# Performance work log

Hardware: AMD Instinct MI355X
Metric: run time of the kernel (lower is better)

## Reference

```python
import jax, jax.numpy as jnp
import numpy as np

B, N_IN, HID, N_OUT = 1024, 512, 64, 256


def setup_inputs() -> dict:
    key = jax.random.key(0)
    ks = jax.random.split(key, 10)
    s = 0.02
    return {
        "x": jax.random.normal(ks[0], (B, N_IN), dtype=jnp.float32),
        "ln_gamma": jnp.ones((N_IN,), dtype=jnp.float32),
        "ln_beta": jnp.zeros((N_IN,), dtype=jnp.float32),
        "Wq": jax.random.normal(ks[1], (N_IN, HID * N_OUT), dtype=jnp.float32) * s,
        "bq": jnp.zeros((HID * N_OUT,), dtype=jnp.float32),
        "Wk": jax.random.normal(ks[2], (N_IN, HID * N_OUT), dtype=jnp.float32) * s,
        "bk": jnp.zeros((HID * N_OUT,), dtype=jnp.float32),
        "Wv": jax.random.normal(ks[3], (N_IN, HID * N_OUT), dtype=jnp.float32) * s,
        "bv": jnp.zeros((HID * N_OUT,), dtype=jnp.float32),
        "Wo": jax.random.normal(ks[4], (HID, N_OUT), dtype=jnp.float32) * s,
        "bo": jnp.zeros((N_OUT,), dtype=jnp.float32),
    }


def reference(x, ln_gamma, ln_beta, Wq, bq, Wk, bk, Wv, bv, Wo, bo):
    # LayerNorm over last dim (input_shape)
    mu = jnp.mean(x, axis=-1, keepdims=True)
    var = jnp.mean(jnp.square(x - mu), axis=-1, keepdims=True)
    h = (x - mu) / jnp.sqrt(var + 1e-5) * ln_gamma + ln_beta  # (B, 512)

    # QKV projections, then view as (B, N_OUT, HID)
    q = (h @ Wq + bq).reshape(B, N_OUT, HID)
    k = (h @ Wk + bk).reshape(B, N_OUT, HID)
    v = (h @ Wv + bv).reshape(B, N_OUT, HID)

    # Single-head scaled dot-product attention over length N_OUT
    w = jnp.einsum("bqc,bkc->bqk", q, k) * (HID ** -0.5)
    w = jax.nn.softmax(w, axis=2)
    a = jnp.einsum("bqk,bkc->bqc", w, v)  # (B, N_OUT, HID)

    # Output projection, ReLU, negate -> seminegative contact map
    out = jax.nn.relu(a @ Wo + bo)  # (B, N_OUT, N_OUT)
    return -out
```

## Files before the change

kernel.cpp:

```cpp
#include <hip/hip_runtime.h>
#include <hip/hip_fp16.h>

typedef _Float16 h4_t __attribute__((ext_vector_type(4)));
typedef _Float16 h8_t __attribute__((ext_vector_type(8)));
typedef float f4_t __attribute__((ext_vector_type(4)));

#define B_SZ 1024
#define N_IN 512
#define HID 64
#define N_OUT 256
#define QKN (N_OUT * HID)

__global__ __launch_bounds__(256) void k_ln(const float* __restrict__ x,
                                            const float* __restrict__ gamma,
                                            const float* __restrict__ beta,
                                            _Float16* __restrict__ h16) {
    int tid = threadIdx.x;
    int wave = tid >> 6, lane = tid & 63;
    int row = blockIdx.x * 4 + wave;
    const float4* xr = (const float4*)(x + (size_t)row * N_IN);
    float4 a = xr[lane];
    float4 b = xr[lane + 64];
    float s = a.x + a.y + a.z + a.w + b.x + b.y + b.z + b.w;
    float sq = a.x * a.x + a.y * a.y + a.z * a.z + a.w * a.w +
               b.x * b.x + b.y * b.y + b.z * b.z + b.w * b.w;
    for (int off = 1; off < 64; off <<= 1) {
        s += __shfl_xor(s, off);
        sq += __shfl_xor(sq, off);
    }
    float mean = s * (1.0f / N_IN);
    float var = sq * (1.0f / N_IN) - mean * mean;
    float rstd = rsqrtf(var + 1e-5f);
    float4 g0 = ((const float4*)gamma)[lane];
    float4 g1 = ((const float4*)gamma)[lane + 64];
    float4 e0 = ((const float4*)beta)[lane];
    float4 e1 = ((const float4*)beta)[lane + 64];
    h4_t o0 = {(_Float16)((a.x - mean) * rstd * g0.x + e0.x),
               (_Float16)((a.y - mean) * rstd * g0.y + e0.y),
               (_Float16)((a.z - mean) * rstd * g0.z + e0.z),
               (_Float16)((a.w - mean) * rstd * g0.w + e0.w)};
    h4_t o1 = {(_Float16)((b.x - mean) * rstd * g1.x + e1.x),
               (_Float16)((b.y - mean) * rstd * g1.y + e1.y),
               (_Float16)((b.z - mean) * rstd * g1.z + e1.z),
               (_Float16)((b.w - mean) * rstd * g1.w + e1.w)};
    h4_t* hr = (h4_t*)(h16 + (size_t)row * N_IN);
    hr[lane] = o0;
    hr[lane + 64] = o1;
}

__global__ __launch_bounds__(256) void k_wt(const float* __restrict__ Wq,
                                            const float* __restrict__ Wk,
                                            const float* __restrict__ Wv,
                                            _Float16* __restrict__ wt) {
    __shared__ _Float16 t[64][65];
    const float* W = blockIdx.z == 0 ? Wq : (blockIdx.z == 1 ? Wk : Wv);
    _Float16* out = wt + (size_t)blockIdx.z * ((size_t)QKN * N_IN);
    int n0 = blockIdx.x * 64, k0 = blockIdx.y * 64;
    int c = threadIdx.x & 63, rq = threadIdx.x >> 6;
    for (int i = 0; i < 16; i++) {
        int r = i * 4 + rq;
        t[r][c] = (_Float16)W[(size_t)(k0 + r) * QKN + n0 + c];
    }
    __syncthreads();
    for (int i = 0; i < 16; i++) {
        int r = i * 4 + rq;
        out[(size_t)(n0 + r) * N_IN + k0 + c] = t[c][r];
    }
}

__global__ __launch_bounds__(256) void k_wo(const float* __restrict__ Wo,
                                            _Float16* __restrict__ wo16) {
    int id = blockIdx.x * 256 + threadIdx.x;
    int hid = id >> 8, no = id & 255;
    wo16[(hid >> 2) * 1024 + no * 4 + (hid & 3)] = (_Float16)Wo[id];
}

__global__ __launch_bounds__(256) void k_qkv(const _Float16* __restrict__ h16,
                                             const _Float16* __restrict__ wt,
                                             const float* __restrict__ bq,
                                             const float* __restrict__ bk,
                                             const float* __restrict__ bv,
                                             _Float16* __restrict__ qkv) {
    __shared__ _Float16 As[128 * 32];
    __shared__ _Float16 Bs[128 * 32];
    int z = blockIdx.z;
    const _Float16* Wb = wt + (size_t)z * ((size_t)QKN * N_IN);
    const float* bias = z == 0 ? bq : (z == 1 ? bk : bv);
    float qscale = (z == 0) ? 0.125f * 1.44269504088896f : 1.0f;
    _Float16* out = qkv + (size_t)z * ((size_t)B_SZ * QKN);
    int m0 = blockIdx.x * 128, n0 = blockIdx.y * 128;
    int tid = threadIdx.x, lane = tid & 63, w = tid >> 6;
    int wm = w & 1, wn = w >> 1;
    int col16 = lane & 15, quad = lane >> 4;
    f4_t acc[4][4] = {};
    for (int kk = 0; kk < N_IN; kk += 32) {
        __syncthreads();
        for (int c = 0; c < 2; c++) {
            int idx = (w * 2 + c) * 512 + lane * 8;
            int row = idx >> 5, col = idx & 31;
            __builtin_amdgcn_global_load_lds(
                (const __attribute__((address_space(1))) void*)(h16 + (size_t)(m0 + row) * N_IN + kk + col),
                (__attribute__((address_space(3))) void*)(As + (w * 2 + c) * 512),
                16, 0, 0);
            __builtin_amdgcn_global_load_lds(
                (const __attribute__((address_space(1))) void*)(Wb + (size_t)(n0 + row) * N_IN + kk + col),
                (__attribute__((address_space(3))) void*)(Bs + (w * 2 + c) * 512),
                16, 0, 0);
        }
        __syncthreads();
        h8_t af[4], bf[4];
        for (int mt = 0; mt < 4; mt++)
            af[mt] = *(const h8_t*)(As + (wm * 64 + mt * 16 + col16) * 32 + quad * 8);
        for (int nt = 0; nt < 4; nt++)
            bf[nt] = *(const h8_t*)(Bs + (wn * 64 + nt * 16 + col16) * 32 + quad * 8);
        for (int mt = 0; mt < 4; mt++)
            for (int nt = 0; nt < 4; nt++)
                acc[mt][nt] = __builtin_amdgcn_mfma_f32_16x16x32_f16(af[mt], bf[nt], acc[mt][nt], 0, 0, 0);
    }
    for (int nt = 0; nt < 4; nt++) {
        int n = n0 + wn * 64 + nt * 16 + col16;
        float bb = bias[n];
        for (int mt = 0; mt < 4; mt++) {
            int mbase = m0 + wm * 64 + mt * 16 + quad * 4;
            for (int r = 0; r < 4; r++)
                out[(size_t)(mbase + r) * QKN + n] = (_Float16)((acc[mt][nt][r] + bb) * qscale);
        }
    }
}

__global__ __launch_bounds__(256, 3) void k_attn(const _Float16* __restrict__ qkv,
                                                 const _Float16* __restrict__ wo16,
                                                 const float* __restrict__ bo,
                                                 float* __restrict__ out) {
    __shared__ _Float16 vt[64 * 258];
    int b = blockIdx.x;
    int tid = threadIdx.x, lane = tid & 63, w = tid >> 6;
    int col16 = lane & 15, quad = lane >> 4;
    const _Float16* qb = qkv + (size_t)b * QKN;
    const _Float16* kb = qkv + (size_t)(B_SZ + b) * QKN;
    const _Float16* vb = qkv + (size_t)(2 * B_SZ + b) * QKN;

    for (int it = 0; it < 4; it++) {
        int id = it * 256 + tid;
        int kg = id & 63, hg = id >> 6;
        h4_t r0 = *(const h4_t*)(vb + (kg * 4 + 0) * 64 + hg * 4);
        h4_t r1 = *(const h4_t*)(vb + (kg * 4 + 1) * 64 + hg * 4);
        h4_t r2 = *(const h4_t*)(vb + (kg * 4 + 2) * 64 + hg * 4);
        h4_t r3 = *(const h4_t*)(vb + (kg * 4 + 3) * 64 + hg * 4);
        for (int j = 0; j < 4; j++) {
            h4_t wv = {r0[j], r1[j], r2[j], r3[j]};
            *(h4_t*)(vt + kg * 258 + (hg * 4 + j) * 4) = wv;
        }
    }

    h8_t qf[4][2];
    int qbase = w * 64;
    for (int qt = 0; qt < 4; qt++)
        for (int ki = 0; ki < 2; ki++)
            qf[qt][ki] = *(const h8_t*)(qb + (size_t)(qbase + qt * 16 + col16) * 64 + ki * 32 + quad * 8);

    __syncthreads();

    f4_t o[4][4] = {};
    float lrun[4] = {0.f, 0.f, 0.f, 0.f};

    for (int kc = 0; kc < 16; kc++) {
        h8_t kf[2];
        for (int ki = 0; ki < 2; ki++)
            kf[ki] = *(const h8_t*)(kb + (size_t)(kc * 16 + col16) * 64 + ki * 32 + quad * 8);
        h4_t vf[4];
        for (int mt = 0; mt < 4; mt++)
            vf[mt] = *(const h4_t*)(vt + (kc * 4 + quad) * 258 + (mt * 16 + col16) * 4);
        for (int qt = 0; qt < 4; qt++) {
            f4_t st = {};
            st = __builtin_amdgcn_mfma_f32_16x16x32_f16(kf[0], qf[qt][0], st, 0, 0, 0);
            st = __builtin_amdgcn_mfma_f32_16x16x32_f16(kf[1], qf[qt][1], st, 0, 0, 0);
            float p0 = exp2f(st[0]), p1 = exp2f(st[1]);
            float p2 = exp2f(st[2]), p3 = exp2f(st[3]);
            lrun[qt] += (p0 + p1) + (p2 + p3);
            h4_t pf = {(_Float16)p0, (_Float16)p1, (_Float16)p2, (_Float16)p3};
            for (int mt = 0; mt < 4; mt++)
                o[mt][qt] = __builtin_amdgcn_mfma_f32_16x16x16f16(vf[mt], pf, o[mt][qt], 0, 0, 0);
        }
    }

    h4_t af[4][4];
    for (int qt = 0; qt < 4; qt++) {
        float l = lrun[qt];
        l += __shfl_xor(l, 16);
        l += __shfl_xor(l, 32);
        float rl = 1.0f / l;
        for (int hk = 0; hk < 4; hk++) {
            f4_t t = o[hk][qt];
            af[qt][hk] = (h4_t){(_Float16)(t[0] * rl), (_Float16)(t[1] * rl),
                                (_Float16)(t[2] * rl), (_Float16)(t[3] * rl)};
        }
    }

    float* outb = out + (size_t)b * (N_OUT * N_OUT);
    for (int nc = 0; nc < 16; nc++) {
        int nb = nc * 16;
        h4_t wf[4];
        for (int hk = 0; hk < 4; hk++)
            wf[hk] = *(const h4_t*)(wo16 + (hk * 4 + quad) * 1024 + (nb + col16) * 4);
        float4 b4 = *(const float4*)(bo + nb + quad * 4);
        for (int qt = 0; qt < 4; qt++) {
            f4_t a = {};
            for (int hk = 0; hk < 4; hk++)
                a = __builtin_amdgcn_mfma_f32_16x16x16f16(wf[hk], af[qt][hk], a, 0, 0, 0);
            float4 res;
            res.x = fminf(-(a[0] + b4.x), 0.f);
            res.y = fminf(-(a[1] + b4.y), 0.f);
            res.z = fminf(-(a[2] + b4.z), 0.f);
            res.w = fminf(-(a[3] + b4.w), 0.f);
            *(float4*)(outb + (size_t)(qbase + qt * 16 + col16) * N_OUT + nb + quad * 4) = res;
        }
    }
}

extern "C" void kernel_launch(void* const* d_in, const int* in_sizes, int n_in,
                              void* d_out, int out_size, void* d_ws, size_t ws_size,
                              hipStream_t stream) {
    const float* x = (const float*)d_in[0];
    const float* gamma = (const float*)d_in[1];
    const float* beta = (const float*)d_in[2];
    const float* Wq = (const float*)d_in[3];
    const float* bq = (const float*)d_in[4];
    const float* Wk = (const float*)d_in[5];
    const float* bk = (const float*)d_in[6];
    const float* Wv = (const float*)d_in[7];
    const float* bv = (const float*)d_in[8];
    const float* Wo = (const float*)d_in[9];
    const float* bo = (const float*)d_in[10];
    float* out = (float*)d_out;

    _Float16* h16 = (_Float16*)d_ws;
    _Float16* wt16 = h16 + (size_t)B_SZ * N_IN;
    _Float16* qkv16 = wt16 + (size_t)3 * QKN * N_IN;
    _Float16* wo16 = qkv16 + (size_t)3 * B_SZ * QKN;

    k_ln<<<dim3(B_SZ / 4), 256, 0, stream>>>(x, gamma, beta, h16);
    k_wo<<<dim3(QKN / 256), 256, 0, stream>>>(Wo, wo16);
    k_wt<<<dim3(QKN / 64, N_IN / 64, 3), 256, 0, stream>>>(Wq, Wk, Wv, wt16);
    k_qkv<<<dim3(B_SZ / 128, QKN / 128, 3), 256, 0, stream>>>(h16, wt16, bq, bk, bv, qkv16);
    k_attn<<<dim3(B_SZ), 256, 0, stream>>>(qkv16, wo16, bo, out);
}
```

Measured before the change: 533.1 us.

## Vectorize weight transpose and QKV epilogue stores, swap grid mapping

The weight transpose kernel now reads float4 rows and writes 4-wide half vectors instead of scalar elements. The QKV GEMM swaps the MFMA operand order, so each lane holds four consecutive output columns. The epilogue can then issue 8-byte vector stores along the contiguous dimension, with float4 bias loads. The grid is also reordered so consecutive blocks walk the N dimension and share the same activation tile. The scalar transposed LDS writes in the transpose kernel may cause more bank conflicts.

```diff
diff --git a/kernel.cpp b/kernel.cpp
--- a/kernel.cpp
+++ b/kernel.cpp
@@ -56,15 +56,26 @@
     const float* W = blockIdx.z == 0 ? Wq : (blockIdx.z == 1 ? Wk : Wv);
     _Float16* out = wt + (size_t)blockIdx.z * ((size_t)QKN * N_IN);
     int n0 = blockIdx.x * 64, k0 = blockIdx.y * 64;
-    int c = threadIdx.x & 63, rq = threadIdx.x >> 6;
-    for (int i = 0; i < 16; i++) {
-        int r = i * 4 + rq;
-        t[r][c] = (_Float16)W[(size_t)(k0 + r) * QKN + n0 + c];
+    int tid = threadIdx.x;
+    {
+        int c4 = tid & 15, r = tid >> 4;
+        for (int i = 0; i < 4; i++) {
+            int kr = i * 16 + r;
+            float4 v = *(const float4*)(W + (size_t)(k0 + kr) * QKN + n0 + c4 * 4);
+            t[c4 * 4 + 0][kr] = (_Float16)v.x;
+            t[c4 * 4 + 1][kr] = (_Float16)v.y;
+            t[c4 * 4 + 2][kr] = (_Float16)v.z;
+            t[c4 * 4 + 3][kr] = (_Float16)v.w;
+        }
     }
     __syncthreads();
-    for (int i = 0; i < 16; i++) {
-        int r = i * 4 + rq;
-        out[(size_t)(n0 + r) * N_IN + k0 + c] = t[c][r];
+    {
+        int n = tid >> 2, kq0 = tid & 3;
+        for (int i = 0; i < 4; i++) {
+            int kq = kq0 + i * 4;
+            h4_t v = *(const h4_t*)(&t[n][kq * 4]);
+            *(h4_t*)(out + (size_t)(n0 + n) * N_IN + k0 + kq * 4) = v;
+        }
     }
 }
 
@@ -88,7 +99,7 @@
     const float* bias = z == 0 ? bq : (z == 1 ? bk : bv);
     float qscale = (z == 0) ? 0.125f * 1.44269504088896f : 1.0f;
     _Float16* out = qkv + (size_t)z * ((size_t)B_SZ * QKN);
-    int m0 = blockIdx.x * 128, n0 = blockIdx.y * 128;
+    int n0 = blockIdx.x * 128, m0 = blockIdx.y * 128;
     int tid = threadIdx.x, lane = tid & 63, w = tid >> 6;
     int wm = w & 1, wn = w >> 1;
     int col16 = lane & 15, quad = lane >> 4;
@@ -115,15 +126,19 @@
             bf[nt] = *(const h8_t*)(Bs + (wn * 64 + nt * 16 + col16) * 32 + quad * 8);
         for (int mt = 0; mt < 4; mt++)
             for (int nt = 0; nt < 4; nt++)
-                acc[mt][nt] = __builtin_amdgcn_mfma_f32_16x16x32_f16(af[mt], bf[nt], acc[mt][nt], 0, 0, 0);
-    }
-    for (int nt = 0; nt < 4; nt++) {
-        int n = n0 + wn * 64 + nt * 16 + col16;
-        float bb = bias[n];
-        for (int mt = 0; mt < 4; mt++) {
-            int mbase = m0 + wm * 64 + mt * 16 + quad * 4;
-            for (int r = 0; r < 4; r++)
-                out[(size_t)(mbase + r) * QKN + n] = (_Float16)((acc[mt][nt][r] + bb) * qscale);
+                acc[mt][nt] = __builtin_amdgcn_mfma_f32_16x16x32_f16(bf[nt], af[mt], acc[mt][nt], 0, 0, 0);
+    }
+    for (int mt = 0; mt < 4; mt++) {
+        size_t m = (size_t)(m0 + wm * 64 + mt * 16 + col16);
+        for (int nt = 0; nt < 4; nt++) {
+            int nb = n0 + wn * 64 + nt * 16 + quad * 4;
+            float4 bb = *(const float4*)(bias + nb);
+            f4_t t = acc[mt][nt];
+            h4_t o4 = {(_Float16)((t[0] + bb.x) * qscale),
+                       (_Float16)((t[1] + bb.y) * qscale),
+                       (_Float16)((t[2] + bb.z) * qscale),
+                       (_Float16)((t[3] + bb.w) * qscale)};
+            *(h4_t*)(out + m * QKN + nb) = o4;
         }
     }
 }
@@ -242,6 +257,6 @@
     k_ln<<<dim3(B_SZ / 4), 256, 0, stream>>>(x, gamma, beta, h16);
     k_wo<<<dim3(QKN / 256), 256, 0, stream>>>(Wo, wo16);
     k_wt<<<dim3(QKN / 64, N_IN / 64, 3), 256, 0, stream>>>(Wq, Wk, Wv, wt16);
-    k_qkv<<<dim3(B_SZ / 128, QKN / 128, 3), 256, 0, stream>>>(h16, wt16, bq, bk, bv, qkv16);
+    k_qkv<<<dim3(QKN / 128, B_SZ / 128, 3), 256, 0, stream>>>(h16, wt16, bq, bk, bv, qkv16);
     k_attn<<<dim3(B_SZ), 256, 0, stream>>>(qkv16, wo16, bo, out);
 }
```

Result: slower. 545.3 us (+2.3%).
